# Kernel optimization log

Measured on AMD Instinct MI355X. Metric: run time of the kernel, lower is better.

## Reference

```python
import jax, jax.numpy as jnp
import numpy as np
import math

V, T, D, N, H, DFF = 32000, 1024, 1024, 6, 16, 4096
DK = D // H
EPS = 1e-6


def setup_inputs() -> dict:
    key = jax.random.key(0)
    ks = jax.random.split(key, 20)
    s = 0.02
    B = 2
    return {
        "idx": jax.random.randint(ks[0], (B, T), 0, V, dtype=jnp.int32),
        "emb": jax.random.normal(ks[1], (V, D), jnp.float32) * s,
        # attention projections, stored [in, out] so y = x @ W
        "Wq": jax.random.normal(ks[2], (N, D, D), jnp.float32) * s,
        "Wk": jax.random.normal(ks[3], (N, D, D), jnp.float32) * s,
        "Wv": jax.random.normal(ks[4], (N, D, D), jnp.float32) * s,
        "Wo": jax.random.normal(ks[5], (N, D, D), jnp.float32) * s,
        "ln1_a": jnp.ones((N, D), jnp.float32),
        "ln1_b": jnp.zeros((N, D), jnp.float32),
        "ln2_a": jnp.ones((N, D), jnp.float32),
        "ln2_b": jnp.zeros((N, D), jnp.float32),
        "W1": jax.random.normal(ks[6], (N, D, DFF), jnp.float32) * s,
        "b1": jnp.zeros((N, DFF), jnp.float32),
        "W2": jax.random.normal(ks[7], (N, DFF, D), jnp.float32) * s,
        "b2": jnp.zeros((N, D), jnp.float32),
        "fnorm_a": jnp.ones((D,), jnp.float32),
        "fnorm_b": jnp.zeros((D,), jnp.float32),
        "Wp": jax.random.normal(ks[8], (D, V), jnp.float32) * s,
        "bp": jnp.zeros((V,), jnp.float32),
    }


def _layernorm(x, a, b):
    # torch .std() uses Bessel correction (ddof=1); denom is (std + eps), not sqrt(var+eps)
    mean = x.mean(axis=-1, keepdims=True)
    std = jnp.std(x, axis=-1, keepdims=True, ddof=1)
    return a * (x - mean) / (std + EPS) + b


def _pos_encoding(t, d):
    pos = jnp.arange(t, dtype=jnp.float32)[:, None]
    div = jnp.exp(jnp.arange(0, d, 2, dtype=jnp.float32) * (-math.log(10000.0) / d))
    pe = jnp.zeros((t, d), jnp.float32)
    pe = pe.at[:, 0::2].set(jnp.sin(pos * div))
    pe = pe.at[:, 1::2].set(jnp.cos(pos * div))
    return pe


def _forward(idx, emb, Wq, Wk, Wv, Wo, ln1_a, ln1_b, ln2_a, ln2_b,
             W1, b1, W2, b2, fnorm_a, fnorm_b, Wp, bp):
    B, Tc = idx.shape
    x = emb[idx] * math.sqrt(D) + _pos_encoding(Tc, D)  # [B,T,D]
    causal = jnp.tril(jnp.ones((Tc, Tc), bool))  # [T,T]

    def block(x, p):
        wq, wk, wv, wo, a1, c1, a2, c2, w1, bb1, w2, bb2 = p
        h_in = _layernorm(x, a1, c1)
        q = (h_in @ wq).reshape(B, Tc, H, DK).transpose(0, 2, 1, 3)
        k = (h_in @ wk).reshape(B, Tc, H, DK).transpose(0, 2, 1, 3)
        v = (h_in @ wv).reshape(B, Tc, H, DK).transpose(0, 2, 1, 3)
        scores = jnp.einsum('bhqd,bhkd->bhqk', q, k) / math.sqrt(DK)
        scores = jnp.where(causal, scores, -1e9)
        attn = jax.nn.softmax(scores, axis=-1)
        o = jnp.einsum('bhqk,bhkd->bhqd', attn, v)
        o = o.transpose(0, 2, 1, 3).reshape(B, Tc, D) @ wo
        x = x + o
        h2 = _layernorm(x, a2, c2)
        ff = jax.nn.relu(h2 @ w1 + bb1) @ w2 + bb2
        x = x + ff
        return x, None

    x, _ = jax.lax.scan(block, x, (Wq, Wk, Wv, Wo, ln1_a, ln1_b, ln2_a, ln2_b, W1, b1, W2, b2))
    x = _layernorm(x, fnorm_a, fnorm_b)
    logits = x @ Wp + bp  # [B,T,V]
    return logits


def reference(idx, emb, Wq, Wk, Wv, Wo, ln1_a, ln1_b, ln2_a, ln2_b,
              W1, b1, W2, b2, fnorm_a, fnorm_b, Wp, bp):
    return _forward(idx, emb, Wq, Wk, Wv, Wo, ln1_a, ln1_b, ln2_a, ln2_b,
                    W1, b1, W2, b2, fnorm_a, fnorm_b, Wp, bp)
```

## Files before the change

### kernel.cpp

```cpp
#include <hip/hip_runtime.h>
#include <hip/hip_bf16.h>
#include <math.h>

#define VOCAB 32000
#define TSEQ 1024
#define DMODEL 1024
#define NLAYERS 6
#define NHEADS 16
#define DFF 4096
#define DKH 64
#define BATCH 2
#define MROWS (BATCH * TSEQ)
#define LN_EPS 1e-6f
#define QKVS 3072

typedef unsigned short u16;
typedef __attribute__((ext_vector_type(8))) short short8v;
typedef __attribute__((ext_vector_type(4))) float f32x4;

__device__ __forceinline__ u16 f2bb(float f) {
    __hip_bfloat16 h = __float2bfloat16(f);
    u16 u; __builtin_memcpy(&u, &h, 2); return u;
}

__device__ __forceinline__ void gload16(const void* g, void* l) {
    __builtin_amdgcn_global_load_lds(
        (const __attribute__((address_space(1))) unsigned int*)g,
        (__attribute__((address_space(3))) unsigned int*)l, 16, 0, 0);
}

__global__ void embed_kernel(const int* __restrict__ idx,
                             const float* __restrict__ emb,
                             float* __restrict__ x) {
    int i = blockIdx.x * blockDim.x + threadIdx.x;
    if (i >= MROWS * DMODEL) return;
    int row = i / DMODEL;
    int d = i - row * DMODEL;
    int t = row % TSEQ;
    int tok = idx[row];
    float e = emb[(size_t)tok * DMODEL + d] * 32.0f;
    float freq = expf(-(float)(d & ~1) * (9.210340371976184f / (float)DMODEL));
    float ang = (float)t * freq;
    float pe = (d & 1) ? cosf(ang) : sinf(ang);
    x[i] = e + pe;
}

template<bool OB16>
__global__ void __launch_bounds__(256) ln_kernel(const float* __restrict__ x,
                                                 const float* __restrict__ a,
                                                 const float* __restrict__ b,
                                                 void* __restrict__ yv) {
    __shared__ float red[8];
    int row = blockIdx.x;
    int tid = threadIdx.x;
    float4 v = ((const float4*)(x + (size_t)row * DMODEL))[tid];
    float s = v.x + v.y + v.z + v.w;
    #pragma unroll
    for (int off = 32; off; off >>= 1) s += __shfl_xor(s, off, 64);
    if ((tid & 63) == 0) red[tid >> 6] = s;
    __syncthreads();
    float mean = (red[0] + red[1] + red[2] + red[3]) * (1.0f / DMODEL);
    float dx = v.x - mean, dy = v.y - mean, dz = v.z - mean, dw = v.w - mean;
    float ss = dx * dx + dy * dy + dz * dz + dw * dw;
    #pragma unroll
    for (int off = 32; off; off >>= 1) ss += __shfl_xor(ss, off, 64);
    if ((tid & 63) == 0) red[4 + (tid >> 6)] = ss;
    __syncthreads();
    float var = (red[4] + red[5] + red[6] + red[7]) * (1.0f / (DMODEL - 1));
    float inv = 1.0f / (sqrtf(var) + LN_EPS);
    const float4 a4 = ((const float4*)a)[tid];
    const float4 b4 = ((const float4*)b)[tid];
    float o0 = a4.x * dx * inv + b4.x;
    float o1 = a4.y * dy * inv + b4.y;
    float o2 = a4.z * dz * inv + b4.z;
    float o3 = a4.w * dw * inv + b4.w;
    if (OB16) {
        ushort4 o; o.x = f2bb(o0); o.y = f2bb(o1); o.z = f2bb(o2); o.w = f2bb(o3);
        ((ushort4*)((u16*)yv + (size_t)row * DMODEL))[tid] = o;
    } else {
        float4 o; o.x = o0; o.y = o1; o.z = o2; o.w = o3;
        ((float4*)((float*)yv + (size_t)row * DMODEL))[tid] = o;
    }
}

__global__ void __launch_bounds__(256) convT(const float* __restrict__ in,
                                             u16* __restrict__ out, int K, int N) {
    __shared__ float t[32][33];
    in  += (size_t)blockIdx.z * K * N;
    out += (size_t)blockIdx.z * K * N;
    const int tx = threadIdx.x, ty = threadIdx.y;
    const int n0 = blockIdx.x * 32, k0 = blockIdx.y * 32;
    #pragma unroll
    for (int i = 0; i < 4; ++i)
        t[ty + i * 8][tx] = in[(size_t)(k0 + ty + i * 8) * N + n0 + tx];
    __syncthreads();
    #pragma unroll
    for (int i = 0; i < 4; ++i)
        out[(size_t)(n0 + ty + i * 8) * K + k0 + tx] = f2bb(t[tx][ty + i * 8]);
}

__global__ void __launch_bounds__(256) convQKVO(const float* __restrict__ Wq,
                                                const float* __restrict__ Wk,
                                                const float* __restrict__ Wv,
                                                const float* __restrict__ Wo,
                                                u16* __restrict__ WqkvT,
                                                u16* __restrict__ WoT) {
    __shared__ float t[32][33];
    const int z = blockIdx.z, L = z >> 2, p = z & 3;
    const size_t MM = (size_t)DMODEL * DMODEL;
    const float* in = (p == 0 ? Wq : p == 1 ? Wk : p == 2 ? Wv : Wo) + (size_t)L * MM;
    u16* out = (p < 3) ? (WqkvT + (size_t)L * 3 * MM + (size_t)p * MM)
                       : (WoT + (size_t)L * MM);
    const int tx = threadIdx.x, ty = threadIdx.y;
    const int n0 = blockIdx.x * 32, k0 = blockIdx.y * 32;
    #pragma unroll
    for (int i = 0; i < 4; ++i)
        t[ty + i * 8][tx] = in[(size_t)(k0 + ty + i * 8) * DMODEL + n0 + tx];
    __syncthreads();
    #pragma unroll
    for (int i = 0; i < 4; ++i)
        out[(size_t)(n0 + ty + i * 8) * DMODEL + k0 + tx] = f2bb(t[tx][ty + i * 8]);
}

template<int BMT, bool BIAS, bool RELU, bool RES, bool OB16>
__global__ void __launch_bounds__(256) gemm_mfma(
    const u16* __restrict__ A, const u16* __restrict__ Bt,
    const float* __restrict__ bias, const float* res,
    void* outp, int N, int K)
{
    constexpr int MR = BMT / 32;
    constexpr int AR = BMT / 64;
    __shared__ u16 Alds[BMT * 32];
    __shared__ u16 Blds[128 * 32];
    const int tid = threadIdx.x;
    const int w = tid >> 6, lane = tid & 63;
    const int wr = w >> 1, wc = w & 1;
    const size_t bm = (size_t)blockIdx.y * BMT;
    const size_t bn = (size_t)blockIdx.x * 128;
    const int srow = (w << 4) + (lane >> 2);
    const int scol = (((lane & 3) ^ ((lane >> 3) & 3)) << 3);
    const int fr = lane & 15, fq = lane >> 4;
    const int aswz = ((fq ^ ((fr >> 1) & 3)) << 3);

    f32x4 acc[MR][4];
    #pragma unroll
    for (int m = 0; m < MR; ++m)
        #pragma unroll
        for (int n = 0; n < 4; ++n)
            acc[m][n] = (f32x4){0.f, 0.f, 0.f, 0.f};

    for (int k0 = 0; k0 < K; k0 += 32) {
        #pragma unroll
        for (int li = 0; li < AR; ++li)
            gload16(A + (bm + li * 64 + srow) * K + k0 + scol, Alds + li * 2048 + w * 512);
        #pragma unroll
        for (int li = 0; li < 2; ++li)
            gload16(Bt + (bn + li * 64 + srow) * K + k0 + scol, Blds + li * 2048 + w * 512);
        __syncthreads();
        short8v a[MR], b[4];
        #pragma unroll
        for (int m = 0; m < MR; ++m)
            a[m] = *(const short8v*)(Alds + (wr * (BMT / 2) + m * 16 + fr) * 32 + aswz);
        #pragma unroll
        for (int n = 0; n < 4; ++n)
            b[n] = *(const short8v*)(Blds + (wc * 64 + n * 16 + fr) * 32 + aswz);
        #pragma unroll
        for (int m = 0; m < MR; ++m)
            #pragma unroll
            for (int n = 0; n < 4; ++n)
                acc[m][n] = __builtin_amdgcn_mfma_f32_16x16x32_bf16(a[m], b[n], acc[m][n], 0, 0, 0);
        __syncthreads();
    }

    #pragma unroll
    for (int n = 0; n < 4; ++n) {
        const size_t col = bn + wc * 64 + n * 16 + fr;
        const float bv = BIAS ? bias[col] : 0.f;
        #pragma unroll
        for (int m = 0; m < MR; ++m) {
            #pragma unroll
            for (int r = 0; r < 4; ++r) {
                const size_t row = bm + wr * (BMT / 2) + m * 16 + fq * 4 + r;
                float v = acc[m][n][r] + bv;
                if (RELU) v = fmaxf(v, 0.f);
                if (RES)  v += res[row * N + col];
                if (OB16) ((u16*)outp)[row * N + col] = f2bb(v);
                else      ((float*)outp)[row * N + col] = v;
            }
        }
    }
}

__global__ void __launch_bounds__(256) attn_flash(const u16* __restrict__ qkv,
                                                  u16* __restrict__ o) {
    __shared__ u16 Klds[32 * 64];
    __shared__ u16 Vt[64 * 32];
    __shared__ u16 Plds[4][16 * 40];

    const int tid = threadIdx.x;
    const int w = tid >> 6, lane = tid & 63;
    const int fr = lane & 15, fq = lane >> 4;
    const int qt = blockIdx.x, h = blockIdx.y, b = blockIdx.z;
    const int qbase = qt * 64 + w * 16;
    const size_t rowbase = (size_t)b * TSEQ;
    const int hd = h * DKH;

    const u16* qrow = qkv + (rowbase + qbase + fr) * QKVS + hd;
    const short8v qf0 = *(const short8v*)(qrow + fq * 8);
    const short8v qf1 = *(const short8v*)(qrow + 32 + fq * 8);

    float m[4], l[4];
    f32x4 oa[4];
    #pragma unroll
    for (int r = 0; r < 4; ++r) { m[r] = -1e30f; l[r] = 0.f; }
    #pragma unroll
    for (int nd = 0; nd < 4; ++nd) oa[nd] = (f32x4){0.f, 0.f, 0.f, 0.f};

    const int ntiles = qt * 2 + 2;
    for (int t = 0; t < ntiles; ++t) {
        const int j0 = t * 32;
        {
            const int r = tid >> 3, c8 = (tid & 7) << 3;
            const size_t grow = (rowbase + j0 + r) * QKVS + hd + c8;
            short8v kv = *(const short8v*)(qkv + grow + 1024);
            int kbyte = (r * 128 + c8 * 2) ^ ((r & 7) << 4);
            *(short8v*)((char*)Klds + kbyte) = kv;
            short8v vv = *(const short8v*)(qkv + grow + 2048);
            #pragma unroll
            for (int i = 0; i < 8; ++i) {
                const int vrow = c8 + i;
                const int chunk = ((r >> 3) + (vrow >> 3)) & 3;
                Vt[vrow * 32 + chunk * 8 + (r & 7)] = (u16)vv[i];
            }
        }
        __syncthreads();

        if (j0 <= qbase + 15) {
            f32x4 s[2];
            #pragma unroll
            for (int ct = 0; ct < 2; ++ct) {
                const int krow = ct * 16 + fr;
                const int swz = (krow & 7) << 4;
                short8v k0 = *(const short8v*)((char*)Klds + ((krow * 128 + fq * 16) ^ swz));
                short8v k1 = *(const short8v*)((char*)Klds + ((krow * 128 + 64 + fq * 16) ^ swz));
                f32x4 a = (f32x4){0.f, 0.f, 0.f, 0.f};
                a = __builtin_amdgcn_mfma_f32_16x16x32_bf16(qf0, k0, a, 0, 0, 0);
                a = __builtin_amdgcn_mfma_f32_16x16x32_bf16(qf1, k1, a, 0, 0, 0);
                s[ct] = a;
            }
            float c[4];
            #pragma unroll
            for (int r = 0; r < 4; ++r) {
                const int qg = qbase + fq * 4 + r;
                float s0 = s[0][r] * 0.125f;
                float s1 = s[1][r] * 0.125f;
                if (j0 + fr      > qg) s0 = -1e30f;
                if (j0 + 16 + fr > qg) s1 = -1e30f;
                float mx = fmaxf(s0, s1);
                mx = fmaxf(mx, __shfl_xor(mx, 1, 64));
                mx = fmaxf(mx, __shfl_xor(mx, 2, 64));
                mx = fmaxf(mx, __shfl_xor(mx, 4, 64));
                mx = fmaxf(mx, __shfl_xor(mx, 8, 64));
                const float mn = fmaxf(m[r], mx);
                c[r] = __expf(m[r] - mn);
                m[r] = mn;
                const float p0 = __expf(s0 - mn);
                const float p1 = __expf(s1 - mn);
                float rs = p0 + p1;
                rs += __shfl_xor(rs, 1, 64);
                rs += __shfl_xor(rs, 2, 64);
                rs += __shfl_xor(rs, 4, 64);
                rs += __shfl_xor(rs, 8, 64);
                l[r] = l[r] * c[r] + rs;
                Plds[w][(fq * 4 + r) * 40 + fr]      = f2bb(p0);
                Plds[w][(fq * 4 + r) * 40 + 16 + fr] = f2bb(p1);
            }
            #pragma unroll
            for (int nd = 0; nd < 4; ++nd)
                #pragma unroll
                for (int r = 0; r < 4; ++r)
                    oa[nd][r] *= c[r];
            asm volatile("s_waitcnt lgkmcnt(0)" ::: "memory");
            __builtin_amdgcn_sched_barrier(0);
            const short8v pf = *(const short8v*)(&Plds[w][fr * 40 + fq * 8]);
            #pragma unroll
            for (int nd = 0; nd < 4; ++nd) {
                const int vrow = nd * 16 + fr;
                const int chunk = (fq + (vrow >> 3)) & 3;
                const short8v vf = *(const short8v*)(&Vt[vrow * 32 + chunk * 8]);
                oa[nd] = __builtin_amdgcn_mfma_f32_16x16x32_bf16(pf, vf, oa[nd], 0, 0, 0);
            }
        }
        __syncthreads();
    }

    #pragma unroll
    for (int r = 0; r < 4; ++r) {
        const float inv = 1.0f / l[r];
        u16* orow = o + (rowbase + qbase + fq * 4 + r) * DMODEL + hd;
        #pragma unroll
        for (int nd = 0; nd < 4; ++nd)
            orow[nd * 16 + fr] = f2bb(oa[nd][r] * inv);
    }
}

#define FBM 64
#define FBN 64
#define FBK 16
__global__ void __launch_bounds__(256) gemm_f32(
    const float* __restrict__ A, const float* __restrict__ Bw,
    const float* __restrict__ bias, float* outp, int N, int K)
{
    __shared__ float As[FBK][FBM];
    __shared__ float Bs[FBK][FBN];
    const int bm = blockIdx.y * FBM, bn = blockIdx.x * FBN;
    const int tid = threadIdx.x;
    const int tr = (tid >> 4) << 2, tc = (tid & 15) << 2;
    const int am = tid >> 2, ak = (tid & 3) << 2;
    const int bk = tid >> 4, bn4 = (tid & 15) << 2;
    float acc[4][4] = {};
    const float* Ap = A + (size_t)(bm + am) * K + ak;
    const float* Bp = Bw + (size_t)bk * N + bn + bn4;
    for (int k0 = 0; k0 < K; k0 += FBK) {
        float4 av = *(const float4*)(Ap + k0);
        float4 bv = *(const float4*)(Bp + (size_t)k0 * N);
        As[ak + 0][am] = av.x; As[ak + 1][am] = av.y; As[ak + 2][am] = av.z; As[ak + 3][am] = av.w;
        *(float4*)&Bs[bk][bn4] = bv;
        __syncthreads();
        #pragma unroll
        for (int kk = 0; kk < FBK; ++kk) {
            float4 a4 = *(const float4*)&As[kk][tr];
            float4 b4 = *(const float4*)&Bs[kk][tc];
            acc[0][0] += a4.x*b4.x; acc[0][1] += a4.x*b4.y; acc[0][2] += a4.x*b4.z; acc[0][3] += a4.x*b4.w;
            acc[1][0] += a4.y*b4.x; acc[1][1] += a4.y*b4.y; acc[1][2] += a4.y*b4.z; acc[1][3] += a4.y*b4.w;
            acc[2][0] += a4.z*b4.x; acc[2][1] += a4.z*b4.y; acc[2][2] += a4.z*b4.z; acc[2][3] += a4.z*b4.w;
            acc[3][0] += a4.w*b4.x; acc[3][1] += a4.w*b4.y; acc[3][2] += a4.w*b4.z; acc[3][3] += a4.w*b4.w;
        }
        __syncthreads();
    }
    #pragma unroll
    for (int i = 0; i < 4; ++i) {
        int row = bm + tr + i;
        float4 o;
        o.x = acc[i][0] + bias[bn + tc + 0];
        o.y = acc[i][1] + bias[bn + tc + 1];
        o.z = acc[i][2] + bias[bn + tc + 2];
        o.w = acc[i][3] + bias[bn + tc + 3];
        *(float4*)(outp + (size_t)row * N + bn + tc) = o;
    }
}

extern "C" void kernel_launch(void* const* d_in, const int* in_sizes, int n_in,
                              void* d_out, int out_size, void* d_ws, size_t ws_size,
                              hipStream_t stream) {
    const int* idx = (const int*)d_in[0];
    const float* emb = (const float*)d_in[1];
    const float* Wq = (const float*)d_in[2];
    const float* Wk = (const float*)d_in[3];
    const float* Wv = (const float*)d_in[4];
    const float* Wo = (const float*)d_in[5];
    const float* ln1a = (const float*)d_in[6];
    const float* ln1b = (const float*)d_in[7];
    const float* ln2a = (const float*)d_in[8];
    const float* ln2b = (const float*)d_in[9];
    const float* W1 = (const float*)d_in[10];
    const float* b1 = (const float*)d_in[11];
    const float* W2 = (const float*)d_in[12];
    const float* b2 = (const float*)d_in[13];
    const float* fa = (const float*)d_in[14];
    const float* fb = (const float*)d_in[15];
    const float* Wp = (const float*)d_in[16];
    const float* bp = (const float*)d_in[17];
    float* out = (float*)d_out;

    const size_t MD = (size_t)MROWS * DMODEL;
    const size_t MM = (size_t)DMODEL * DMODEL;
    u16* U = (u16*)out;
    u16* qkv = U;
    u16* ob = U + 3 * MD;
    u16* hb = U + 4 * MD;
    float* x = (float*)(U + 5 * MD);
    u16* ff = U + 7 * MD;
    u16* WqkvT = U + 12 * MD;
    u16* WoT = U + 21 * MD;
    u16* W1T = U + 24 * MD;
    u16* W2T = U + 36 * MD;

    const bool pathA = ws_size >= (size_t)68 * 1024 * 1024 + 256;
    u16* WpT = (u16*)d_ws;
    u16* h2b = (u16*)((char*)d_ws + (size_t)64 * 1024 * 1024);
    float* hF = (float*)d_ws;

    dim3 cblk(32, 8);
    convQKVO<<<dim3(32, 32, 24), cblk, 0, stream>>>(Wq, Wk, Wv, Wo, WqkvT, WoT);
    convT<<<dim3(128, 32, 6), cblk, 0, stream>>>(W1, W1T, DMODEL, DFF);
    convT<<<dim3(32, 128, 6), cblk, 0, stream>>>(W2, W2T, DFF, DMODEL);
    if (pathA) convT<<<dim3(1000, 32, 1), cblk, 0, stream>>>(Wp, WpT, DMODEL, VOCAB);

    embed_kernel<<<(MROWS * DMODEL + 255) / 256, 256, 0, stream>>>(idx, emb, x);

    for (int L = 0; L < NLAYERS; ++L) {
        ln_kernel<true><<<MROWS, 256, 0, stream>>>(x, ln1a + (size_t)L * DMODEL, ln1b + (size_t)L * DMODEL, hb);
        gemm_mfma<128, false, false, false, true><<<dim3(24, 16), 256, 0, stream>>>(
            hb, WqkvT + (size_t)L * 3 * MM, nullptr, nullptr, qkv, QKVS, DMODEL);
        attn_flash<<<dim3(TSEQ / 64, NHEADS, BATCH), 256, 0, stream>>>(qkv, ob);
        gemm_mfma<64, false, false, true, false><<<dim3(8, 32), 256, 0, stream>>>(
            ob, WoT + (size_t)L * MM, nullptr, x, x, DMODEL, DMODEL);
        ln_kernel<true><<<MROWS, 256, 0, stream>>>(x, ln2a + (size_t)L * DMODEL, ln2b + (size_t)L * DMODEL, hb);
        gemm_mfma<128, true, true, false, true><<<dim3(32, 16), 256, 0, stream>>>(
            hb, W1T + (size_t)L * DFF * DMODEL, b1 + (size_t)L * DFF, nullptr, ff, DFF, DMODEL);
        gemm_mfma<64, true, false, true, false><<<dim3(8, 32), 256, 0, stream>>>(
            ff, W2T + (size_t)L * DFF * DMODEL, b2 + (size_t)L * DMODEL, x, x, DMODEL, DFF);
    }

    if (pathA) {
        ln_kernel<true><<<MROWS, 256, 0, stream>>>(x, fa, fb, h2b);
        gemm_mfma<128, true, false, false, false><<<dim3(250, 16), 256, 0, stream>>>(
            h2b, WpT, bp, nullptr, out, VOCAB, DMODEL);
    } else {
        ln_kernel<false><<<MROWS, 256, 0, stream>>>(x, fa, fb, hF);
        gemm_f32<<<dim3(VOCAB / FBN, MROWS / FBM), 256, 0, stream>>>(hF, Wp, bp, out, VOCAB, DMODEL);
    }
}
```

Measured before the change: 1.840 ms.

## Widen attention KV tiles to 64, add MFMA priority hints, enlarge vocab GEMM tile

The attention kernel now processes 64-key tiles per iteration instead of 32. This halves the loop trips and barriers and drops the per-wave causal skip branch. s_setprio hints are wrapped around the MFMA bursts in both the GEMM and attention kernels so waves doing math get scheduling priority. The final vocab projection uses a 256-row M tile with half as many row blocks, for more reuse of the weight tile. The costs are more LDS and registers per block, and some fully masked work on diagonal tiles for the lower waves.

```diff
diff --git a/kernel.cpp b/kernel.cpp
--- a/kernel.cpp
+++ b/kernel.cpp
@@ -164,11 +164,13 @@
         #pragma unroll
         for (int n = 0; n < 4; ++n)
             b[n] = *(const short8v*)(Blds + (wc * 64 + n * 16 + fr) * 32 + aswz);
+        __builtin_amdgcn_s_setprio(1);
         #pragma unroll
         for (int m = 0; m < MR; ++m)
             #pragma unroll
             for (int n = 0; n < 4; ++n)
                 acc[m][n] = __builtin_amdgcn_mfma_f32_16x16x32_bf16(a[m], b[n], acc[m][n], 0, 0, 0);
+        __builtin_amdgcn_s_setprio(0);
         __syncthreads();
     }
 
@@ -193,9 +195,9 @@
 
 __global__ void __launch_bounds__(256) attn_flash(const u16* __restrict__ qkv,
                                                   u16* __restrict__ o) {
-    __shared__ u16 Klds[32 * 64];
-    __shared__ u16 Vt[64 * 32];
-    __shared__ u16 Plds[4][16 * 40];
+    __shared__ u16 Klds[64 * 64];
+    __shared__ u16 Vt[64 * 64];
+    __shared__ u16 Plds[4][16 * 72];
 
     const int tid = threadIdx.x;
     const int w = tid >> 6, lane = tid & 63;
@@ -216,11 +218,12 @@
     #pragma unroll
     for (int nd = 0; nd < 4; ++nd) oa[nd] = (f32x4){0.f, 0.f, 0.f, 0.f};
 
-    const int ntiles = qt * 2 + 2;
-    for (int t = 0; t < ntiles; ++t) {
-        const int j0 = t * 32;
-        {
-            const int r = tid >> 3, c8 = (tid & 7) << 3;
+    for (int t = 0; t <= qt; ++t) {
+        const int j0 = t * 64;
+        #pragma unroll
+        for (int half = 0; half < 2; ++half) {
+            const int r = (tid >> 3) + half * 32;
+            const int c8 = (tid & 7) << 3;
             const size_t grow = (rowbase + j0 + r) * QKVS + hd + c8;
             short8v kv = *(const short8v*)(qkv + grow + 1024);
             int kbyte = (r * 128 + c8 * 2) ^ ((r & 7) << 4);
@@ -229,68 +232,82 @@
             #pragma unroll
             for (int i = 0; i < 8; ++i) {
                 const int vrow = c8 + i;
-                const int chunk = ((r >> 3) + (vrow >> 3)) & 3;
-                Vt[vrow * 32 + chunk * 8 + (r & 7)] = (u16)vv[i];
+                const int slot = ((r >> 3) + (vrow >> 3)) & 7;
+                Vt[vrow * 64 + slot * 8 + (r & 7)] = (u16)vv[i];
             }
         }
         __syncthreads();
 
-        if (j0 <= qbase + 15) {
-            f32x4 s[2];
-            #pragma unroll
-            for (int ct = 0; ct < 2; ++ct) {
-                const int krow = ct * 16 + fr;
-                const int swz = (krow & 7) << 4;
-                short8v k0 = *(const short8v*)((char*)Klds + ((krow * 128 + fq * 16) ^ swz));
-                short8v k1 = *(const short8v*)((char*)Klds + ((krow * 128 + 64 + fq * 16) ^ swz));
-                f32x4 a = (f32x4){0.f, 0.f, 0.f, 0.f};
-                a = __builtin_amdgcn_mfma_f32_16x16x32_bf16(qf0, k0, a, 0, 0, 0);
-                a = __builtin_amdgcn_mfma_f32_16x16x32_bf16(qf1, k1, a, 0, 0, 0);
-                s[ct] = a;
+        f32x4 s[4];
+        __builtin_amdgcn_s_setprio(1);
+        #pragma unroll
+        for (int ct = 0; ct < 4; ++ct) {
+            const int krow = ct * 16 + fr;
+            const int swz = (krow & 7) << 4;
+            short8v k0 = *(const short8v*)((char*)Klds + ((krow * 128 + fq * 16) ^ swz));
+            short8v k1 = *(const short8v*)((char*)Klds + ((krow * 128 + 64 + fq * 16) ^ swz));
+            f32x4 a = (f32x4){0.f, 0.f, 0.f, 0.f};
+            a = __builtin_amdgcn_mfma_f32_16x16x32_bf16(qf0, k0, a, 0, 0, 0);
+            a = __builtin_amdgcn_mfma_f32_16x16x32_bf16(qf1, k1, a, 0, 0, 0);
+            s[ct] = a;
+        }
+        __builtin_amdgcn_s_setprio(0);
+
+        float c[4];
+        #pragma unroll
+        for (int r = 0; r < 4; ++r) {
+            const int qg = qbase + fq * 4 + r;
+            float sv[4];
+            #pragma unroll
+            for (int ct = 0; ct < 4; ++ct) {
+                sv[ct] = s[ct][r] * 0.125f;
+                if (j0 + ct * 16 + fr > qg) sv[ct] = -1e30f;
             }
-            float c[4];
-            #pragma unroll
-            for (int r = 0; r < 4; ++r) {
-                const int qg = qbase + fq * 4 + r;
-                float s0 = s[0][r] * 0.125f;
-                float s1 = s[1][r] * 0.125f;
-                if (j0 + fr      > qg) s0 = -1e30f;
-                if (j0 + 16 + fr > qg) s1 = -1e30f;
-                float mx = fmaxf(s0, s1);
-                mx = fmaxf(mx, __shfl_xor(mx, 1, 64));
-                mx = fmaxf(mx, __shfl_xor(mx, 2, 64));
-                mx = fmaxf(mx, __shfl_xor(mx, 4, 64));
-                mx = fmaxf(mx, __shfl_xor(mx, 8, 64));
-                const float mn = fmaxf(m[r], mx);
-                c[r] = __expf(m[r] - mn);
-                m[r] = mn;
-                const float p0 = __expf(s0 - mn);
-                const float p1 = __expf(s1 - mn);
-                float rs = p0 + p1;
-                rs += __shfl_xor(rs, 1, 64);
-                rs += __shfl_xor(rs, 2, 64);
-                rs += __shfl_xor(rs, 4, 64);
-                rs += __shfl_xor(rs, 8, 64);
-                l[r] = l[r] * c[r] + rs;
-                Plds[w][(fq * 4 + r) * 40 + fr]      = f2bb(p0);
-                Plds[w][(fq * 4 + r) * 40 + 16 + fr] = f2bb(p1);
-            }
-            #pragma unroll
-            for (int nd = 0; nd < 4; ++nd)
-                #pragma unroll
-                for (int r = 0; r < 4; ++r)
-                    oa[nd][r] *= c[r];
-            asm volatile("s_waitcnt lgkmcnt(0)" ::: "memory");
-            __builtin_amdgcn_sched_barrier(0);
-            const short8v pf = *(const short8v*)(&Plds[w][fr * 40 + fq * 8]);
+            float mx = fmaxf(fmaxf(sv[0], sv[1]), fmaxf(sv[2], sv[3]));
+            mx = fmaxf(mx, __shfl_xor(mx, 1, 64));
+            mx = fmaxf(mx, __shfl_xor(mx, 2, 64));
+            mx = fmaxf(mx, __shfl_xor(mx, 4, 64));
+            mx = fmaxf(mx, __shfl_xor(mx, 8, 64));
+            const float mn = fmaxf(m[r], mx);
+            c[r] = __expf(m[r] - mn);
+            m[r] = mn;
+            float p0 = __expf(sv[0] - mn);
+            float p1 = __expf(sv[1] - mn);
+            float p2 = __expf(sv[2] - mn);
+            float p3 = __expf(sv[3] - mn);
+            float rs = (p0 + p1) + (p2 + p3);
+            rs += __shfl_xor(rs, 1, 64);
+            rs += __shfl_xor(rs, 2, 64);
+            rs += __shfl_xor(rs, 4, 64);
+            rs += __shfl_xor(rs, 8, 64);
+            l[r] = l[r] * c[r] + rs;
+            u16* prow = &Plds[w][(fq * 4 + r) * 72];
+            prow[fr]      = f2bb(p0);
+            prow[16 + fr] = f2bb(p1);
+            prow[32 + fr] = f2bb(p2);
+            prow[48 + fr] = f2bb(p3);
+        }
+        #pragma unroll
+        for (int nd = 0; nd < 4; ++nd)
+            #pragma unroll
+            for (int r = 0; r < 4; ++r)
+                oa[nd][r] *= c[r];
+        asm volatile("s_waitcnt lgkmcnt(0)" ::: "memory");
+        __builtin_amdgcn_sched_barrier(0);
+
+        __builtin_amdgcn_s_setprio(1);
+        #pragma unroll
+        for (int ks = 0; ks < 2; ++ks) {
+            const short8v pf = *(const short8v*)(&Plds[w][fr * 72 + ks * 32 + fq * 8]);
             #pragma unroll
             for (int nd = 0; nd < 4; ++nd) {
                 const int vrow = nd * 16 + fr;
-                const int chunk = (fq + (vrow >> 3)) & 3;
-                const short8v vf = *(const short8v*)(&Vt[vrow * 32 + chunk * 8]);
+                const int slot = (ks * 4 + fq + (vrow >> 3)) & 7;
+                const short8v vf = *(const short8v*)(&Vt[vrow * 64 + slot * 8]);
                 oa[nd] = __builtin_amdgcn_mfma_f32_16x16x32_bf16(pf, vf, oa[nd], 0, 0, 0);
             }
         }
+        __builtin_amdgcn_s_setprio(0);
         __syncthreads();
     }
 
@@ -415,7 +432,7 @@
 
     if (pathA) {
         ln_kernel<true><<<MROWS, 256, 0, stream>>>(x, fa, fb, h2b);
-        gemm_mfma<128, true, false, false, false><<<dim3(250, 16), 256, 0, stream>>>(
+        gemm_mfma<256, true, false, false, false><<<dim3(250, 8), 256, 0, stream>>>(
             h2b, WpT, bp, nullptr, out, VOCAB, DMODEL);
     } else {
         ln_kernel<false><<<MROWS, 256, 0, stream>>>(x, fa, fb, hF);
```

Measured after the change: 1.870 ms. About the same (+1.6%).
